# Kernel optimization log

Hardware: AMD Instinct MI355X
Metric: run time of the kernel (lower is better)

The kernel has to match this reference:

```python
import jax, jax.numpy as jnp
import numpy as np

B, S_DEC, S_ENC, D, H = 2, 2048, 2048, 1024, 16
HD = D // H  # 64


def setup_inputs() -> dict:
    key = jax.random.key(0)
    ks = jax.random.split(key, 12)
    s = 0.02
    return {
        "dec_hidden_state": jax.random.normal(ks[0], (B, S_DEC, D), jnp.float32),
        "enc_hidden_state": jax.random.normal(ks[1], (B, S_ENC, D), jnp.float32),
        "mask": jnp.ones((B, S_ENC, S_DEC), jnp.int32),
        "Wq": jax.random.normal(ks[2], (H, D, HD), jnp.float32) * s,
        "bq": jax.random.normal(ks[3], (H, HD), jnp.float32) * s,
        "Wk": jax.random.normal(ks[4], (H, D, HD), jnp.float32) * s,
        "bk": jax.random.normal(ks[5], (H, HD), jnp.float32) * s,
        "Wv": jax.random.normal(ks[6], (H, D, HD), jnp.float32) * s,
        "bv": jax.random.normal(ks[7], (H, HD), jnp.float32) * s,
        "Wo": jax.random.normal(ks[8], (D, D), jnp.float32) * s,
        "bo": jax.random.normal(ks[9], (D,), jnp.float32) * s,
    }


def reference(dec_hidden_state, enc_hidden_state, mask, Wq, bq, Wk, bk, Wv, bv, Wo, bo):
    # NOTE: original module swaps args: query <- enc_hidden_state, key/value <- dec_hidden_state.
    # q: [B,H,S_enc,HD], k/v: [B,H,S_dec,HD]
    q = jnp.einsum("bqd,hdk->bhqk", enc_hidden_state, Wq) + bq[None, :, None, :]
    k = jnp.einsum("bsd,hdk->bhsk", dec_hidden_state, Wk) + bk[None, :, None, :]
    v = jnp.einsum("bsd,hdk->bhsk", dec_hidden_state, Wv) + bv[None, :, None, :]
    scores = jnp.einsum("bhqk,bhsk->bhqs", q, k) / jnp.sqrt(jnp.asarray(HD, q.dtype))
    scores = jnp.where(mask[:, None, :, :] == 0, jnp.asarray(-jnp.inf, scores.dtype), scores)
    weights = jax.nn.softmax(scores, axis=-1)
    attn = jnp.einsum("bhqs,bhsk->bhqk", weights, v)  # [B,H,S_enc,HD]
    # concat heads along last dim (same order as torch.cat over head list)
    attn = jnp.transpose(attn, (0, 2, 1, 3)).reshape(B, S_ENC, D)
    return attn @ Wo + bo
```

## Files before the change

kernel.cpp:

```cpp
#include <hip/hip_runtime.h>
#include <math.h>
#include <stdint.h>


typedef unsigned short ushort_t;
typedef __attribute__((ext_vector_type(8))) short short8;
typedef __attribute__((ext_vector_type(4))) short short4v;
typedef __attribute__((ext_vector_type(4))) float floatx4;

__device__ __forceinline__ ushort_t f2bf(float x){
  unsigned u = __float_as_uint(x);
  u += 0x7fffu + ((u >> 16) & 1u);
  return (ushort_t)(u >> 16);
}
__device__ __forceinline__ unsigned pk2bf(float a, float b){
#if __has_builtin(__builtin_amdgcn_cvt_pk_bf16_f32)
  typedef __attribute__((ext_vector_type(2))) __bf16 bf2_t;
  bf2_t r = __builtin_amdgcn_cvt_pk_bf16_f32(a, b);
  return *(unsigned*)&r;
#else
  return (unsigned)f2bf(a) | ((unsigned)f2bf(b) << 16);
#endif
}
__device__ __forceinline__ floatx4 mfma16(short8 a, short8 b, floatx4 c){
  return __builtin_amdgcn_mfma_f32_16x16x32_bf16(a, b, c, 0, 0, 0);
}
#if __has_builtin(__builtin_amdgcn_mfma_f32_16x16x16bf16_1k)
__device__ __forceinline__ floatx4 mfma_pv(short4v a, short4v b, floatx4 c){
  return __builtin_amdgcn_mfma_f32_16x16x16bf16_1k(a, b, c, 0, 0, 0);
}
#else
__device__ __forceinline__ floatx4 mfma_pv(short4v a, short4v b, floatx4 c){
  short8 a8 = {a[0], a[1], a[2], a[3], 0, 0, 0, 0};
  short8 b8 = {b[0], b[1], b[2], b[3], 0, 0, 0, 0};
  return mfma16(a8, b8, c);
}
#endif

__global__ __launch_bounds__(256)
void prep_kernel(const float* __restrict__ enc, const float* __restrict__ dec,
                 const float* __restrict__ Wq, const float* __restrict__ Wk,
                 const float* __restrict__ Wv, const float* __restrict__ Wo,
                 const int* __restrict__ mask,
                 ushort_t* __restrict__ encb, ushort_t* __restrict__ decb,
                 ushort_t* __restrict__ WqT, ushort_t* __restrict__ WkT,
                 ushort_t* __restrict__ WvT, ushort_t* __restrict__ WoT,
                 unsigned long long* __restrict__ mb)
{
  __shared__ float t[64][65];
  const int bx = blockIdx.x, tid = threadIdx.x;
  if (bx < 8192){
    const float* src = (bx < 4096) ? enc : dec;
    ushort_t*    dst = (bx < 4096) ? encb : decb;
    int i = ((bx & 4095) * 256 + tid) * 4;
    const float4 v = *(const float4*)(src + i);
    unsigned long long p = (unsigned long long)f2bf(v.x)
                         | ((unsigned long long)f2bf(v.y) << 16)
                         | ((unsigned long long)f2bf(v.z) << 32)
                         | ((unsigned long long)f2bf(v.w) << 48);
    *(unsigned long long*)(dst + i) = p;
  } else if (bx < 8960){
    const int id = bx - 8192;
    const int zz = id >> 4, yy = id & 15;
    const int which = zz >> 4, head = zz & 15;
    const float* src = (which == 0) ? Wq : (which == 1) ? Wk : Wv;
    ushort_t*    dst = (which == 0) ? WqT : (which == 1) ? WkT : WvT;
    const long sb = (long)head * 65536;
    const int r0 = yy * 64;
    #pragma unroll
    for (int i = 0; i < 16; i++){
      int idx = i*256 + tid;
      int r = idx >> 6, c = idx & 63;
      t[r][c] = src[sb + (long)(r0 + r)*64 + c];
    }
    __syncthreads();
    #pragma unroll
    for (int i = 0; i < 16; i++){
      int idx = i*256 + tid;
      int cr = idx >> 6, rc = idx & 63;
      dst[sb + (long)cr*1024 + r0 + rc] = f2bf(t[rc][cr]);
    }
  } else if (bx < 9216){
    const int id = bx - 8960;
    const int r0 = (id >> 4) * 64, c0 = (id & 15) * 64;
    #pragma unroll
    for (int i = 0; i < 16; i++){
      int idx = i*256 + tid;
      int r = idx >> 6, c = idx & 63;
      t[r][c] = Wo[(long)(r0 + r)*1024 + c0 + c];
    }
    __syncthreads();
    #pragma unroll
    for (int i = 0; i < 16; i++){
      int idx = i*256 + tid;
      int cr = idx >> 6, rc = idx & 63;
      WoT[(long)(c0 + cr)*1024 + r0 + rc] = f2bf(t[rc][cr]);
    }
  } else {
    long gid = (long)(bx - 9216) * 256 + tid;
    unsigned long long bal = __ballot(mask[gid] != 0);
    if ((tid & 63) == 0) mb[gid >> 6] = bal;
  }
}

__global__ __launch_bounds__(256, 3)
void gemm_qkv_kernel(const ushort_t* __restrict__ encb, const ushort_t* __restrict__ decb,
                     const ushort_t* __restrict__ WqT, const ushort_t* __restrict__ WkT,
                     const ushort_t* __restrict__ WvT,
                     const float* __restrict__ bq, const float* __restrict__ bk,
                     const float* __restrict__ bv,
                     ushort_t* __restrict__ Qb, ushort_t* __restrict__ Kbf,
                     ushort_t* __restrict__ Vtb)
{
  __shared__ ushort_t At[2*4096];
  __shared__ ushort_t Bt[2*4096];
  const int tid = threadIdx.x;
  const int wave = tid >> 6, lane = tid & 63;
  const int quad = lane >> 4, l16 = lane & 15;
  const int z = blockIdx.z;
  const ushort_t *A, *BT; const float* bias; ushort_t* outp;
  int m0, n0; long outAdj = 0;
  float qs = 1.0f;
  if (z == 0){ A = encb; BT = WqT; bias = bq; outp = Qb;  m0 = blockIdx.x*128; n0 = blockIdx.y*128;
               qs = 0.18033688011112042f; }
  else if (z == 1){ A = decb; BT = WkT; bias = bk; outp = Kbf; m0 = blockIdx.x*128; n0 = blockIdx.y*128; }
  else {
    int id = blockIdx.x*8 + blockIdx.y;
    int vb = id >> 7, rem = id & 127;
    m0 = ((rem >> 4) & 7) * 128; n0 = (rem & 15) * 128;
    A = WvT; BT = decb + (long)vb*2097152; bias = bv; outp = Vtb; outAdj = (long)vb*2097152;
  }
  const int K = 1024;

  const int c0 = tid, c1 = 256 + tid;
  const ushort_t* gA0 = A  + (long)(m0 + (c0 >> 2))*K + (c0 & 3)*8;
  const ushort_t* gA1 = A  + (long)(m0 + (c1 >> 2))*K + (c1 & 3)*8;
  const ushort_t* gB0 = BT + (long)(n0 + (c0 >> 2))*K + (c0 & 3)*8;
  const ushort_t* gB1 = BT + (long)(n0 + (c1 >> 2))*K + (c1 & 3)*8;

  floatx4 acc[4][4];
  #pragma unroll
  for (int mt = 0; mt < 4; mt++)
    #pragma unroll
    for (int nt = 0; nt < 4; nt++)
      acc[mt][nt] = (floatx4){0.f, 0.f, 0.f, 0.f};

  short8 rA0 = *(const short8*)gA0;  gA0 += 32;
  short8 rA1 = *(const short8*)gA1;  gA1 += 32;
  short8 rB0 = *(const short8*)gB0;  gB0 += 32;
  short8 rB1 = *(const short8*)gB1;  gB1 += 32;

  const int moff = (wave & 1) * 64, noff = (wave >> 1) * 64;
  int cur = 0;
  for (int k0 = 0; k0 < K; k0 += 32){
    *(short8*)&At[cur*4096 +        tid*8] = rA0;
    *(short8*)&At[cur*4096 + 2048 + tid*8] = rA1;
    *(short8*)&Bt[cur*4096 +        tid*8] = rB0;
    *(short8*)&Bt[cur*4096 + 2048 + tid*8] = rB1;
    __syncthreads();
    if (k0 + 32 < K){
      rA0 = *(const short8*)gA0;  gA0 += 32;
      rA1 = *(const short8*)gA1;  gA1 += 32;
      rB0 = *(const short8*)gB0;  gB0 += 32;
      rB1 = *(const short8*)gB1;  gB1 += 32;
    }
    short8 af[4], bfr[4];
    #pragma unroll
    for (int t = 0; t < 4; t++){
      af[t]  = *(const short8*)&At[cur*4096 + (moff + t*16 + l16)*32 + quad*8];
      bfr[t] = *(const short8*)&Bt[cur*4096 + (noff + t*16 + l16)*32 + quad*8];
    }
    #pragma unroll
    for (int mt = 0; mt < 4; mt++)
      #pragma unroll
      for (int nt = 0; nt < 4; nt++)
        acc[mt][nt] = mfma16(bfr[nt], af[mt], acc[mt][nt]);
    cur ^= 1;
  }

  #pragma unroll
  for (int mt = 0; mt < 4; mt++){
    #pragma unroll
    for (int nt = 0; nt < 4; nt++){
      floatx4 v = acc[mt][nt];
      if (z < 2){
        const int s   = m0 + moff + mt*16 + l16;
        const int ch0 = n0 + noff + nt*16 + quad*4;
        const float4 b4 = *(const float4*)&bias[ch0];
        uint2 pk;
        pk.x = pk2bf((v[0] + b4.x)*qs, (v[1] + b4.y)*qs);
        pk.y = pk2bf((v[2] + b4.z)*qs, (v[3] + b4.w)*qs);
        *(unsigned long long*)&outp[(long)s*1024 + ch0] = *(unsigned long long*)&pk;
      } else {
        const int ch = m0 + moff + mt*16 + l16;
        const int s0 = n0 + noff + nt*16 + quad*4;
        const float bb = bias[ch];
        uint2 pk;
        pk.x = pk2bf(v[0] + bb, v[1] + bb);
        pk.y = pk2bf(v[2] + bb, v[3] + bb);
        *(unsigned long long*)&outp[outAdj + (long)ch*2048 + s0] = *(unsigned long long*)&pk;
      }
    }
  }
}

__global__ __launch_bounds__(256, 2)
void gemm_o_kernel(const ushort_t* __restrict__ A, const ushort_t* __restrict__ BT,
                   const float* __restrict__ bias, float* __restrict__ outf)
{
  __shared__ ushort_t At[2*4096];
  __shared__ ushort_t Bt[2*2048];
  const int tid = threadIdx.x;
  const int wave = tid >> 6, lane = tid & 63;
  const int quad = lane >> 4, l16 = lane & 15;
  const int m0 = blockIdx.x * 128, n0 = blockIdx.y * 64;
  const int K = 1024;

  const int c0 = tid, c1 = 256 + tid;
  const ushort_t* gA0 = A  + (long)(m0 + (c0 >> 2))*K + (c0 & 3)*8;
  const ushort_t* gA1 = A  + (long)(m0 + (c1 >> 2))*K + (c1 & 3)*8;
  const ushort_t* gB0 = BT + (long)(n0 + (c0 >> 2))*K + (c0 & 3)*8;

  floatx4 acc[4][2];
  #pragma unroll
  for (int mt = 0; mt < 4; mt++)
    #pragma unroll
    for (int nt = 0; nt < 2; nt++)
      acc[mt][nt] = (floatx4){0.f, 0.f, 0.f, 0.f};

  short8 rA0 = *(const short8*)gA0;  gA0 += 32;
  short8 rA1 = *(const short8*)gA1;  gA1 += 32;
  short8 rB0 = *(const short8*)gB0;  gB0 += 32;

  const int moff = (wave & 1) * 64, noff = (wave >> 1) * 32;
  int cur = 0;
  for (int k0 = 0; k0 < K; k0 += 32){
    *(short8*)&At[cur*4096 +        tid*8] = rA0;
    *(short8*)&At[cur*4096 + 2048 + tid*8] = rA1;
    *(short8*)&Bt[cur*2048 +        tid*8] = rB0;
    __syncthreads();
    if (k0 + 32 < K){
      rA0 = *(const short8*)gA0;  gA0 += 32;
      rA1 = *(const short8*)gA1;  gA1 += 32;
      rB0 = *(const short8*)gB0;  gB0 += 32;
    }
    short8 af[4], bfr[2];
    #pragma unroll
    for (int t = 0; t < 4; t++)
      af[t]  = *(const short8*)&At[cur*4096 + (moff + t*16 + l16)*32 + quad*8];
    #pragma unroll
    for (int t = 0; t < 2; t++)
      bfr[t] = *(const short8*)&Bt[cur*2048 + (noff + t*16 + l16)*32 + quad*8];
    #pragma unroll
    for (int mt = 0; mt < 4; mt++)
      #pragma unroll
      for (int nt = 0; nt < 2; nt++)
        acc[mt][nt] = mfma16(bfr[nt], af[mt], acc[mt][nt]);
    cur ^= 1;
  }

  #pragma unroll
  for (int mt = 0; mt < 4; mt++){
    #pragma unroll
    for (int nt = 0; nt < 2; nt++){
      const int s   = m0 + moff + mt*16 + l16;
      const int ch0 = n0 + noff + nt*16 + quad*4;
      const float4 b4 = *(const float4*)&bias[ch0];
      float4 o;
      o.x = acc[mt][nt][0] + b4.x;
      o.y = acc[mt][nt][1] + b4.y;
      o.z = acc[mt][nt][2] + b4.z;
      o.w = acc[mt][nt][3] + b4.w;
      *(float4*)&outf[(long)s*1024 + ch0] = o;
    }
  }
}

__global__ __launch_bounds__(256, 2)
void flash_attn_kernel(const ushort_t* __restrict__ Qp, const ushort_t* __restrict__ Kp,
                       const ushort_t* __restrict__ Vt, const unsigned* __restrict__ mb,
                       ushort_t* __restrict__ aout)
{
  __shared__ ushort_t Kbuf[2*4608];
  __shared__ ushort_t Vbuf[2*4608];
  const int tid = threadIdx.x, wave = tid >> 6, lane = tid & 63;
  const int quad = lane >> 4, l16 = lane & 15;
  const int bh = blockIdx.x, qt = blockIdx.y;
  const int b = bh >> 4, h = bh & 15;

  const ushort_t* VB = Vt + (long)bh*131072;
  const int q0 = qt*128 + wave*32;

  short8 qf[2][2];
  #pragma unroll
  for (int mtq = 0; mtq < 2; mtq++){
    const long qrow = ((long)b*2048 + q0 + mtq*16 + l16)*1024 + h*64;
    qf[mtq][0] = *(const short8*)&Qp[qrow +      quad*8];
    qf[mtq][1] = *(const short8*)&Qp[qrow + 32 + quad*8];
  }

  floatx4 accO[2][4];
  #pragma unroll
  for (int mtq = 0; mtq < 2; mtq++)
    #pragma unroll
    for (int ht = 0; ht < 4; ht++) accO[mtq][ht] = (floatx4){0.f,0.f,0.f,0.f};
  float lsum[2] = {0.f, 0.f};

  const int c0 = tid, c1 = 256 + tid;
  const ushort_t* gK0 = Kp + ((long)b*2048 + (c0 >> 3))*1024 + h*64 + (c0 & 7)*8;
  const ushort_t* gK1 = Kp + ((long)b*2048 + (c1 >> 3))*1024 + h*64 + (c1 & 7)*8;
  const ushort_t* gV0 = VB + (long)(c0 >> 3)*2048 + (c0 & 7)*8;
  const ushort_t* gV1 = VB + (long)(c1 >> 3)*2048 + (c1 & 7)*8;
  const int lo0 = (c0 >> 3)*72 + (c0 & 7)*8;
  const int lo1 = (c1 >> 3)*72 + (c1 & 7)*8;

  const uint2* mb2 = (const uint2*)mb;
  const long mbase = (long)b*2048 + q0;

  short8 gk0 = *(const short8*)gK0;  gK0 += 65536;
  short8 gk1 = *(const short8*)gK1;  gK1 += 65536;
  short8 gv0 = *(const short8*)gV0;  gV0 += 64;
  short8 gv1 = *(const short8*)gV1;  gV1 += 64;

  int cur = 0;
  for (int st = 0; st < 32; st++){
    *(short8*)&Kbuf[cur*4608 + lo0] = gk0;
    *(short8*)&Kbuf[cur*4608 + lo1] = gk1;
    *(short8*)&Vbuf[cur*4608 + lo0] = gv0;
    *(short8*)&Vbuf[cur*4608 + lo1] = gv1;
    __syncthreads();
    if (st < 31){
      gk0 = *(const short8*)gK0;  gK0 += 65536;
      gk1 = *(const short8*)gK1;  gK1 += 65536;
      gv0 = *(const short8*)gV0;  gV0 += 64;
      gv1 = *(const short8*)gV1;  gV1 += 64;
    }
    const ushort_t* Kt = &Kbuf[cur*4608];
    const ushort_t* Vp = &Vbuf[cur*4608];

    uint2 mw[2];
    #pragma unroll
    for (int mtq = 0; mtq < 2; mtq++)
      mw[mtq] = mb2[(mbase + mtq*16 + l16)*32 + st];
    const bool uni = __all((mw[0].x & mw[0].y & mw[1].x & mw[1].y) == 0xFFFFFFFFu);

    #pragma unroll
    for (int mtile = 0; mtile < 4; mtile++){
      short8 kf0 = *(const short8*)&Kt[(mtile*16 + l16)*72 +      quad*8];
      short8 kf1 = *(const short8*)&Kt[(mtile*16 + l16)*72 + 32 + quad*8];
      short4v vf[4];
      #pragma unroll
      for (int ht = 0; ht < 4; ht++)
        vf[ht] = *(const short4v*)&Vp[(ht*16 + l16)*72 + mtile*16 + quad*4];
      #pragma unroll
      for (int mtq = 0; mtq < 2; mtq++){
        floatx4 zz = (floatx4){0.f,0.f,0.f,0.f};
        zz = mfma16(kf0, qf[mtq][0], zz);
        zz = mfma16(kf1, qf[mtq][1], zz);
        float p0 = __builtin_amdgcn_exp2f(zz[0]);
        float p1 = __builtin_amdgcn_exp2f(zz[1]);
        float p2 = __builtin_amdgcn_exp2f(zz[2]);
        float p3 = __builtin_amdgcn_exp2f(zz[3]);
        if (__builtin_expect(!uni, 0)){
          const unsigned w = (mtile & 2) ? mw[mtq].y : mw[mtq].x;
          const int sh = (mtile & 1)*16 + quad*4;
          p0 = ((w >> (sh+0)) & 1u) ? p0 : 0.f;
          p1 = ((w >> (sh+1)) & 1u) ? p1 : 0.f;
          p2 = ((w >> (sh+2)) & 1u) ? p2 : 0.f;
          p3 = ((w >> (sh+3)) & 1u) ? p3 : 0.f;
        }
        lsum[mtq] += (p0 + p1) + (p2 + p3);
        uint2 pk; pk.x = pk2bf(p0, p1); pk.y = pk2bf(p2, p3);
        const short4v pb = *(const short4v*)&pk;
        #pragma unroll
        for (int ht = 0; ht < 4; ht++)
          accO[mtq][ht] = mfma_pv(vf[ht], pb, accO[mtq][ht]);
      }
    }
    cur ^= 1;
  }

  #pragma unroll
  for (int mtq = 0; mtq < 2; mtq++){
    lsum[mtq] += __shfl_xor(lsum[mtq], 16);
    lsum[mtq] += __shfl_xor(lsum[mtq], 32);
  }

  #pragma unroll
  for (int mtq = 0; mtq < 2; mtq++){
    const float inv = 1.0f / lsum[mtq];
    const long rowo = ((long)b*2048 + q0 + mtq*16 + l16)*1024 + h*64;
    #pragma unroll
    for (int ht = 0; ht < 4; ht++){
      uint2 pk;
      pk.x = pk2bf(accO[mtq][ht][0]*inv, accO[mtq][ht][1]*inv);
      pk.y = pk2bf(accO[mtq][ht][2]*inv, accO[mtq][ht][3]*inv);
      *(unsigned long long*)&aout[rowo + ht*16 + quad*4] = *(unsigned long long*)&pk;
    }
  }
}

extern "C" void kernel_launch(void* const* d_in, const int* in_sizes, int n_in,
                              void* d_out, int out_size, void* d_ws, size_t ws_size,
                              hipStream_t stream) {
  const float* dec  = (const float*)d_in[0];
  const float* enc  = (const float*)d_in[1];
  const int*   mask = (const int*)d_in[2];
  const float* Wq   = (const float*)d_in[3];
  const float* bq   = (const float*)d_in[4];
  const float* Wk   = (const float*)d_in[5];
  const float* bk   = (const float*)d_in[6];
  const float* Wv   = (const float*)d_in[7];
  const float* bv   = (const float*)d_in[8];
  const float* Wo   = (const float*)d_in[9];
  const float* bo   = (const float*)d_in[10];
  float* out = (float*)d_out;

  ushort_t* ws   = (ushort_t*)d_ws;
  ushort_t* encb = ws;
  ushort_t* decb = encb + 4194304;
  ushort_t* Qb   = decb + 4194304;
  ushort_t* Kbf  = Qb   + 4194304;
  ushort_t* Vtb  = Kbf  + 4194304;
  ushort_t* WqT  = Vtb  + 4194304;
  ushort_t* WkT  = WqT  + 1048576;
  ushort_t* WvT  = WkT  + 1048576;
  ushort_t* WoT  = WvT  + 1048576;
  unsigned* Mb   = (unsigned*)(WoT + 1048576);

  prep_kernel<<<41984, 256, 0, stream>>>(enc, dec, Wq, Wk, Wv, Wo, mask,
                                         encb, decb, WqT, WkT, WvT, WoT,
                                         (unsigned long long*)Mb);
  gemm_qkv_kernel<<<dim3(32,8,3), 256, 0, stream>>>(encb, decb, WqT, WkT, WvT,
                                                    bq, bk, bv, Qb, Kbf, Vtb);
  flash_attn_kernel<<<dim3(32,16,1), 256, 0, stream>>>(Qb, Kbf, Vtb, Mb, encb);
  gemm_o_kernel<<<dim3(32,16,1), 256, 0, stream>>>(encb, WoT, bo, out);
}
```

Before: 258.0 us.

## Use 16x16x32 MFMA for PV by permuting K rows in shared memory

K tiles are now stored in LDS with a permuted row order, so two score tiles computed by the 16x16x32 MFMA yield a lane layout that forms a full 8-element bf16 P operand. The PV product then uses the wider 16x16x32 bf16 MFMA instead of the 16x16x16 variant, halving the number of PV MFMA instructions and using 8-wide V fragment loads. Mask bit indexing is remapped to match the permutation. This adds some index arithmetic and register pressure, and correctness depends on the permutation matching the MFMA output layout.

```diff
diff --git a/kernel.cpp b/kernel.cpp
--- a/kernel.cpp
+++ b/kernel.cpp
@@ -5,7 +5,6 @@
 
 typedef unsigned short ushort_t;
 typedef __attribute__((ext_vector_type(8))) short short8;
-typedef __attribute__((ext_vector_type(4))) short short4v;
 typedef __attribute__((ext_vector_type(4))) float floatx4;
 
 __device__ __forceinline__ ushort_t f2bf(float x){
@@ -25,17 +24,6 @@
 __device__ __forceinline__ floatx4 mfma16(short8 a, short8 b, floatx4 c){
   return __builtin_amdgcn_mfma_f32_16x16x32_bf16(a, b, c, 0, 0, 0);
 }
-#if __has_builtin(__builtin_amdgcn_mfma_f32_16x16x16bf16_1k)
-__device__ __forceinline__ floatx4 mfma_pv(short4v a, short4v b, floatx4 c){
-  return __builtin_amdgcn_mfma_f32_16x16x16bf16_1k(a, b, c, 0, 0, 0);
-}
-#else
-__device__ __forceinline__ floatx4 mfma_pv(short4v a, short4v b, floatx4 c){
-  short8 a8 = {a[0], a[1], a[2], a[3], 0, 0, 0, 0};
-  short8 b8 = {b[0], b[1], b[2], b[3], 0, 0, 0, 0};
-  return mfma16(a8, b8, c);
-}
-#endif
 
 __global__ __launch_bounds__(256)
 void prep_kernel(const float* __restrict__ enc, const float* __restrict__ dec,
@@ -307,12 +295,17 @@
   float lsum[2] = {0.f, 0.f};
 
   const int c0 = tid, c1 = 256 + tid;
-  const ushort_t* gK0 = Kp + ((long)b*2048 + (c0 >> 3))*1024 + h*64 + (c0 & 7)*8;
-  const ushort_t* gK1 = Kp + ((long)b*2048 + (c1 >> 3))*1024 + h*64 + (c1 & 7)*8;
-  const ushort_t* gV0 = VB + (long)(c0 >> 3)*2048 + (c0 & 7)*8;
-  const ushort_t* gV1 = VB + (long)(c1 >> 3)*2048 + (c1 & 7)*8;
-  const int lo0 = (c0 >> 3)*72 + (c0 & 7)*8;
-  const int lo1 = (c1 >> 3)*72 + (c1 & 7)*8;
+  const int sr0 = c0 >> 3, sr1 = c1 >> 3;
+  const int kr0 = (sr0 & 32) + ((sr0 & 4) << 2) + ((sr0 >> 3) & 3)*4 + (sr0 & 3);
+  const int kr1 = (sr1 & 32) + ((sr1 & 4) << 2) + ((sr1 >> 3) & 3)*4 + (sr1 & 3);
+  const ushort_t* gK0 = Kp + ((long)b*2048 + sr0)*1024 + h*64 + (c0 & 7)*8;
+  const ushort_t* gK1 = Kp + ((long)b*2048 + sr1)*1024 + h*64 + (c1 & 7)*8;
+  const ushort_t* gV0 = VB + (long)sr0*2048 + (c0 & 7)*8;
+  const ushort_t* gV1 = VB + (long)sr1*2048 + (c1 & 7)*8;
+  const int ko0 = kr0*72 + (c0 & 7)*8;
+  const int ko1 = kr1*72 + (c1 & 7)*8;
+  const int vo0 = sr0*72 + (c0 & 7)*8;
+  const int vo1 = sr1*72 + (c1 & 7)*8;
 
   const uint2* mb2 = (const uint2*)mb;
   const long mbase = (long)b*2048 + q0;
@@ -324,10 +317,10 @@
 
   int cur = 0;
   for (int st = 0; st < 32; st++){
-    *(short8*)&Kbuf[cur*4608 + lo0] = gk0;
-    *(short8*)&Kbuf[cur*4608 + lo1] = gk1;
-    *(short8*)&Vbuf[cur*4608 + lo0] = gv0;
-    *(short8*)&Vbuf[cur*4608 + lo1] = gv1;
+    *(short8*)&Kbuf[cur*4608 + ko0] = gk0;
+    *(short8*)&Kbuf[cur*4608 + ko1] = gk1;
+    *(short8*)&Vbuf[cur*4608 + vo0] = gv0;
+    *(short8*)&Vbuf[cur*4608 + vo1] = gv1;
     __syncthreads();
     if (st < 31){
       gk0 = *(const short8*)gK0;  gK0 += 65536;
@@ -345,36 +338,55 @@
     const bool uni = __all((mw[0].x & mw[0].y & mw[1].x & mw[1].y) == 0xFFFFFFFFu);
 
     #pragma unroll
-    for (int mtile = 0; mtile < 4; mtile++){
-      short8 kf0 = *(const short8*)&Kt[(mtile*16 + l16)*72 +      quad*8];
-      short8 kf1 = *(const short8*)&Kt[(mtile*16 + l16)*72 + 32 + quad*8];
-      short4v vf[4];
+    for (int c = 0; c < 2; c++){
+      short8 kA0 = *(const short8*)&Kt[((c*2    )*16 + l16)*72 +      quad*8];
+      short8 kA1 = *(const short8*)&Kt[((c*2    )*16 + l16)*72 + 32 + quad*8];
+      short8 kB0 = *(const short8*)&Kt[((c*2 + 1)*16 + l16)*72 +      quad*8];
+      short8 kB1 = *(const short8*)&Kt[((c*2 + 1)*16 + l16)*72 + 32 + quad*8];
+      short8 vf[4];
       #pragma unroll
       for (int ht = 0; ht < 4; ht++)
-        vf[ht] = *(const short4v*)&Vp[(ht*16 + l16)*72 + mtile*16 + quad*4];
+        vf[ht] = *(const short8*)&Vp[(ht*16 + l16)*72 + c*32 + quad*8];
+
       #pragma unroll
       for (int mtq = 0; mtq < 2; mtq++){
-        floatx4 zz = (floatx4){0.f,0.f,0.f,0.f};
-        zz = mfma16(kf0, qf[mtq][0], zz);
-        zz = mfma16(kf1, qf[mtq][1], zz);
-        float p0 = __builtin_amdgcn_exp2f(zz[0]);
-        float p1 = __builtin_amdgcn_exp2f(zz[1]);
-        float p2 = __builtin_amdgcn_exp2f(zz[2]);
-        float p3 = __builtin_amdgcn_exp2f(zz[3]);
+        floatx4 zA = (floatx4){0.f,0.f,0.f,0.f};
+        zA = mfma16(kA0, qf[mtq][0], zA);
+        zA = mfma16(kA1, qf[mtq][1], zA);
+        floatx4 zB = (floatx4){0.f,0.f,0.f,0.f};
+        zB = mfma16(kB0, qf[mtq][0], zB);
+        zB = mfma16(kB1, qf[mtq][1], zB);
+        float pA0 = __builtin_amdgcn_exp2f(zA[0]);
+        float pA1 = __builtin_amdgcn_exp2f(zA[1]);
+        float pA2 = __builtin_amdgcn_exp2f(zA[2]);
+        float pA3 = __builtin_amdgcn_exp2f(zA[3]);
+        float pB0 = __builtin_amdgcn_exp2f(zB[0]);
+        float pB1 = __builtin_amdgcn_exp2f(zB[1]);
+        float pB2 = __builtin_amdgcn_exp2f(zB[2]);
+        float pB3 = __builtin_amdgcn_exp2f(zB[3]);
         if (__builtin_expect(!uni, 0)){
-          const unsigned w = (mtile & 2) ? mw[mtq].y : mw[mtq].x;
-          const int sh = (mtile & 1)*16 + quad*4;
-          p0 = ((w >> (sh+0)) & 1u) ? p0 : 0.f;
-          p1 = ((w >> (sh+1)) & 1u) ? p1 : 0.f;
-          p2 = ((w >> (sh+2)) & 1u) ? p2 : 0.f;
-          p3 = ((w >> (sh+3)) & 1u) ? p3 : 0.f;
+          const unsigned w = c ? mw[mtq].y : mw[mtq].x;
+          const int sh = quad*8;
+          pA0 = ((w >> (sh+0)) & 1u) ? pA0 : 0.f;
+          pA1 = ((w >> (sh+1)) & 1u) ? pA1 : 0.f;
+          pA2 = ((w >> (sh+2)) & 1u) ? pA2 : 0.f;
+          pA3 = ((w >> (sh+3)) & 1u) ? pA3 : 0.f;
+          pB0 = ((w >> (sh+4)) & 1u) ? pB0 : 0.f;
+          pB1 = ((w >> (sh+5)) & 1u) ? pB1 : 0.f;
+          pB2 = ((w >> (sh+6)) & 1u) ? pB2 : 0.f;
+          pB3 = ((w >> (sh+7)) & 1u) ? pB3 : 0.f;
         }
-        lsum[mtq] += (p0 + p1) + (p2 + p3);
-        uint2 pk; pk.x = pk2bf(p0, p1); pk.y = pk2bf(p2, p3);
-        const short4v pb = *(const short4v*)&pk;
+        lsum[mtq] += ((pA0 + pA1) + (pA2 + pA3)) + ((pB0 + pB1) + (pB2 + pB3));
+        unsigned pk[4];
+        pk[0] = pk2bf(pA0, pA1);
+        pk[1] = pk2bf(pA2, pA3);
+        pk[2] = pk2bf(pB0, pB1);
+        pk[3] = pk2bf(pB2, pB3);
+        short8 pb;
+        __builtin_memcpy(&pb, pk, 16);
         #pragma unroll
         for (int ht = 0; ht < 4; ht++)
-          accO[mtq][ht] = mfma_pv(vf[ht], pb, accO[mtq][ht]);
+          accO[mtq][ht] = mfma16(vf[ht], pb, accO[mtq][ht]);
       }
     }
     cur ^= 1;
```

Result: faster. 247.1 us (-4.2%).
